# Kernel optimization log

Hardware: AMD Instinct MI355X
Metric: run time of the kernel (lower is better)

The kernel has to match this reference:

```python
import jax, jax.numpy as jnp
import numpy as np

N, C, K, P, Q, PS = 32, 128, 128, 64, 64, 3

def setup_inputs() -> dict:
    key = jax.random.key(0)
    k1, k2, k3 = jax.random.split(key, 3)
    x = jax.random.normal(k1, (N, C, P, Q), dtype=jnp.float32)
    W = jax.random.normal(k2, (K, C * PS * PS), dtype=jnp.float32) * (1.0 / np.sqrt(C * PS * PS))
    perturbs = jax.random.normal(k3, (N, K, P, Q), dtype=jnp.float32)
    return {"x": x, "W": W, "perturbs": perturbs}

def reference(x, W, perturbs):
    # patchify (pad=1, unfold 3x3, stride 1) + matmul with W^T is exactly a
    # 3x3 SAME convolution: flatten order of patchify is (C, kh, kw), matching
    # conv.weight.reshape(k, -1). Express it as a direct conv (no im2col blowup).
    k = W.shape[0]
    c = x.shape[1]
    w = W.reshape(k, c, PS, PS)  # OIHW
    out = jax.lax.conv_general_dilated(
        x, w,
        window_strides=(1, 1),
        padding=((1, 1), (1, 1)),
        dimension_numbers=("NCHW", "OIHW", "NCHW"),
    )
    return out + perturbs
```

## Files before the change

### kernel.cpp

```cpp
#include <hip/hip_runtime.h>
#include <hip/hip_bf16.h>

#define NN 32
#define CCH 128
#define KK 128
#define PP 64
#define QQ 64

typedef __bf16 bf16x8 __attribute__((ext_vector_type(8)));
typedef float f32x16 __attribute__((ext_vector_type(16)));
typedef float f32x4 __attribute__((ext_vector_type(4)));

#define XT_ELEMS (32ull * 64 * 64 * 128)

__global__ __launch_bounds__(256) void prep_x(const float* __restrict__ x,
                                              __bf16* __restrict__ xT) {
    __shared__ float tile[128 * 64];
    const int t = threadIdx.x;
    const int p = blockIdx.x;
    const int n = blockIdx.y;

#pragma unroll
    for (int pass = 0; pass < 8; ++pass) {
        int idx = pass * 256 + t;
        int qf = idx & 15;
        int c  = idx >> 4;
        f32x4 v = *(const f32x4*)(x + (((size_t)n * CCH + c) * PP + p) * QQ + qf * 4);
        int key = ((c >> 3) & 15) * 4;
        *(f32x4*)(tile + c * 64 + ((qf * 4) ^ key)) = v;
    }
    __syncthreads();

#pragma unroll
    for (int pass = 0; pass < 4; ++pass) {
        int cc   = pass * 2 + (t >> 7);
        int rem  = t & 127;
        int q    = rem >> 1;
        int half = rem & 1;
        int c0   = cc * 16 + half * 8;
        int key  = ((c0 >> 3) & 15) * 4;
        bf16x8 o;
#pragma unroll
        for (int j = 0; j < 8; ++j) o[j] = (__bf16)tile[(c0 + j) * 64 + (q ^ key)];
        *(bf16x8*)(xT + ((((size_t)n * 8 + cc) * PP + p) * QQ + q) * 16 + half * 8) = o;
    }
}

__global__ __launch_bounds__(256) void prep_w(const float* __restrict__ W,
                                              __bf16* __restrict__ Wf) {
    const int id = blockIdx.x * 256 + threadIdx.x;
    const int lane = id & 63;
    const int r1   = id >> 6;
    const int kb   = r1 & 3;
    const int r2   = r1 >> 2;
    const int t    = r2 % 9;
    const int cc   = r2 / 9;

    const int k  = kb * 32 + (lane & 31);
    const int c0 = cc * 16 + (lane >> 5) * 8;

    bf16x8 o;
#pragma unroll
    for (int j = 0; j < 8; ++j)
        o[j] = (__bf16)W[(size_t)k * (CCH * 9) + (size_t)(c0 + j) * 9 + t];
    ((bf16x8*)Wf)[id] = o;
}

__global__ __launch_bounds__(256, 2) void conv_main(const __bf16* __restrict__ xT,
                                                    const __bf16* __restrict__ Wf,
                                                    const float* __restrict__ per,
                                                    float* __restrict__ out) {
    __shared__ __align__(16) char scr_lds[4][4096];

    const int tid  = threadIdx.x;
    const int lane = tid & 63;
    const int w    = tid >> 6;
    const int kbs  = w & 1;
    const int pb   = w >> 1;
    const int n    = blockIdx.y;
    const int p0   = blockIdx.x * 4;
    const int m    = lane & 31;
    const int half = lane >> 5;

    bf16x8 bz;
#pragma unroll
    for (int j = 0; j < 8; ++j) bz[j] = (__bf16)0.f;

    f32x16 acc[2][2][2];
#pragma unroll
    for (int a = 0; a < 2; ++a)
#pragma unroll
        for (int b = 0; b < 2; ++b)
#pragma unroll
            for (int c = 0; c < 2; ++c)
#pragma unroll
                for (int e = 0; e < 16; ++e) acc[a][b][c][e] = 0.f;

    const char* xb = (const char*)xT + ((size_t)n * 8) * PP * QQ * 32;

    const bf16x8* wg = (const bf16x8*)Wf + kbs * 128 + lane;

    auto compute = [&](int cc) {
        const char* xcc = xb + (size_t)cc * (PP * QQ * 32);
        const bf16x8* wc = wg + (size_t)cc * 2304;

        bf16x8 a_cur[3][2], a_prev[3][2];
#pragma unroll
        for (int ri = 0; ri < 4; ++ri) {
            const int r  = p0 + pb * 2 + ri - 1;
            const bool rok = ((unsigned)r < (unsigned)PP);

            bf16x8 b[3][2];
            if (rok) {
                const char* xrow = xcc + (size_t)r * 2048 + half * 16;
#pragma unroll
                for (int dq = 0; dq < 3; ++dq)
#pragma unroll
                    for (int qb = 0; qb < 2; ++qb) {
                        int q_in = qb * 32 + m + dq - 1;
                        bool ok  = ((unsigned)q_in < (unsigned)QQ);
                        int qc   = ok ? q_in : 0;
                        bf16x8 v = *(const bf16x8*)(xrow + qc * 32);
                        b[dq][qb] = ok ? v : bz;
                    }
            }

            if (ri < 3) {
#pragma unroll
                for (int dq = 0; dq < 3; ++dq)
#pragma unroll
                    for (int kb = 0; kb < 2; ++kb)
                        a_cur[dq][kb] = wc[((ri * 3 + dq) * 4 + kb) * 64];
            }

            if (rok) {
                if (ri >= 1) {
#pragma unroll
                    for (int dq = 0; dq < 3; ++dq)
#pragma unroll
                        for (int kb = 0; kb < 2; ++kb)
#pragma unroll
                            for (int qb = 0; qb < 2; ++qb)
                                acc[1][kb][qb] = __builtin_amdgcn_mfma_f32_32x32x16_bf16(
                                    a_prev[dq][kb], b[dq][qb], acc[1][kb][qb], 0, 0, 0);
                }
                if (ri < 3) {
#pragma unroll
                    for (int dq = 0; dq < 3; ++dq)
#pragma unroll
                        for (int kb = 0; kb < 2; ++kb)
#pragma unroll
                            for (int qb = 0; qb < 2; ++qb)
                                acc[0][kb][qb] = __builtin_amdgcn_mfma_f32_32x32x16_bf16(
                                    a_cur[dq][kb], b[dq][qb], acc[0][kb][qb], 0, 0, 0);
                }
            }

            if (ri < 3) {
#pragma unroll
                for (int dq = 0; dq < 3; ++dq)
#pragma unroll
                    for (int kb = 0; kb < 2; ++kb) a_prev[dq][kb] = a_cur[dq][kb];
            }
        }
    };

    for (int cc = 0; cc < 7; ++cc) compute(cc);

    auto tile_addr = [&](int it, int j) -> size_t {
        int oi = it >> 2, kbi = (it >> 1) & 1, qb = it & 1;
        int prow = p0 + pb * 2 + oi;
        int k = (kbs * 2 + kbi) * 32 + (lane >> 3) + j * 8;
        int q = qb * 32 + (lane & 7) * 4;
        return (((size_t)n * KK + k) * PP + prow) * QQ + q;
    };

    float* scr = (float*)scr_lds[w];

    auto process = [&](int it, f32x4 (&pv)[4]) {
        int oi = it >> 2, kbi = (it >> 1) & 1, qb = it & 1;
        f32x16 v = acc[oi][kbi][qb];
#pragma unroll
        for (int r = 0; r < 16; ++r) {
            int kl = (r & 3) + 8 * (r >> 2) + 4 * half;
            scr[kl * 32 + ((((m >> 2) ^ (kl & 7)) << 2) | (m & 3))] = v[r];
        }
#pragma unroll
        for (int j = 0; j < 4; ++j) {
            int kl = (lane >> 3) + j * 8;
            f32x4 d = *(const f32x4*)(scr + kl * 32 + (((lane & 7) ^ (kl & 7)) << 2));
            f32x4 s = d + pv[j];
            __builtin_nontemporal_store(s, (f32x4*)(out + tile_addr(it, j)));
        }
    };

    f32x4 pv0[4], pv1[4];
#pragma unroll
    for (int j = 0; j < 4; ++j) pv0[j] = *(const f32x4*)(per + tile_addr(0, j));

    compute(7);

#pragma unroll
    for (int itp = 0; itp < 4; ++itp) {
        const int itA = itp * 2, itB = itp * 2 + 1;
#pragma unroll
        for (int j = 0; j < 4; ++j) pv1[j] = *(const f32x4*)(per + tile_addr(itB, j));
        process(itA, pv0);
        if (itp < 3) {
#pragma unroll
            for (int j = 0; j < 4; ++j)
                pv0[j] = *(const f32x4*)(per + tile_addr(itA + 2, j));
        }
        process(itB, pv1);
    }
}

extern "C" void kernel_launch(void* const* d_in, const int* in_sizes, int n_in,
                              void* d_out, int out_size, void* d_ws, size_t ws_size,
                              hipStream_t stream) {
    const float* x   = (const float*)d_in[0];
    const float* W   = (const float*)d_in[1];
    const float* per = (const float*)d_in[2];
    float* out = (float*)d_out;

    __bf16* xT = (__bf16*)d_ws;
    __bf16* Wf = (__bf16*)((char*)d_ws + XT_ELEMS * 2);

    prep_x<<<dim3(PP, NN), 256, 0, stream>>>(x, xT);
    prep_w<<<dim3(72), 256, 0, stream>>>(W, Wf);
    conv_main<<<dim3(PP / 4, NN), 256, 0, stream>>>(xT, Wf, per, out);
}
```

Baseline: 214.6 us.

## Stage input rows in LDS via async global-to-LDS loads, halve rows per block

The conv kernel now stages four channel chunks of the 4 input rows it needs (with zeroed halo columns) into LDS using global_load_lds, and reads B fragments from LDS instead of with per-lane bounds-checked global loads. Each block now covers 2 output rows instead of 4, so the grid doubles, the per-wave accumulators halve, and occupancy is raised to 3 blocks per CU. The aim is to remove the column-boundary select logic and redundant global traffic and to lower register pressure. In exchange it adds block-wide barriers between staging and compute with no overlap, and the 3-row halo is reloaded for every 2 output rows.

```diff
diff --git a/kernel.cpp b/kernel.cpp
--- a/kernel.cpp
+++ b/kernel.cpp
@@ -66,11 +66,16 @@
     ((bf16x8*)Wf)[id] = o;
 }
 
-__global__ __launch_bounds__(256, 2) void conv_main(const __bf16* __restrict__ xT,
+#define XPITCH 2112
+#define XROWS  4
+#define CC_HALF 4
+#define XLDS_BYTES (CC_HALF * XROWS * XPITCH)
+
+__global__ __launch_bounds__(256, 3) void conv_main(const __bf16* __restrict__ xT,
                                                     const __bf16* __restrict__ Wf,
                                                     const float* __restrict__ per,
                                                     float* __restrict__ out) {
-    __shared__ __align__(16) char scr_lds[4][4096];
+    __shared__ __align__(16) char xlds[XLDS_BYTES];
 
     const int tid  = threadIdx.x;
     const int lane = tid & 63;
@@ -78,108 +83,107 @@
     const int kbs  = w & 1;
     const int pb   = w >> 1;
     const int n    = blockIdx.y;
-    const int p0   = blockIdx.x * 4;
+    const int p0   = blockIdx.x * 2;
     const int m    = lane & 31;
     const int half = lane >> 5;
 
-    bf16x8 bz;
-#pragma unroll
-    for (int j = 0; j < 8; ++j) bz[j] = (__bf16)0.f;
-
-    f32x16 acc[2][2][2];
-#pragma unroll
-    for (int a = 0; a < 2; ++a)
-#pragma unroll
-        for (int b = 0; b < 2; ++b)
-#pragma unroll
-            for (int c = 0; c < 2; ++c)
-#pragma unroll
-                for (int e = 0; e < 16; ++e) acc[a][b][c][e] = 0.f;
+    if (tid < 64) {
+        int row = tid >> 2, part = tid & 3;
+        int off = row * XPITCH + (part >> 1) * 2080 + (part & 1) * 16;
+        *(f32x4*)(xlds + off) = f32x4{0.f, 0.f, 0.f, 0.f};
+    }
+
+    f32x16 acc[2][2];
+#pragma unroll
+    for (int b = 0; b < 2; ++b)
+#pragma unroll
+        for (int c = 0; c < 2; ++c)
+#pragma unroll
+            for (int e = 0; e < 16; ++e) acc[b][c][e] = 0.f;
 
     const char* xb = (const char*)xT + ((size_t)n * 8) * PP * QQ * 32;
 
+    auto stage4 = [&](int ccb) {
+#pragma unroll
+        for (int it = 0; it < 8; ++it) {
+            int id  = it * 256 + tid;
+            int cc4 = id >> 9;
+            int rem = id & 511;
+            int row = rem >> 7;
+            int wi  = (rem & 127) * 16;
+            int r   = p0 - 1 + row;
+            int rc  = r < 0 ? 0 : (r > 63 ? 63 : r);
+            __builtin_amdgcn_global_load_lds(
+                (const __attribute__((address_space(1))) unsigned int*)
+                    (xb + (size_t)(ccb + cc4) * 131072 + (size_t)rc * 2048 + wi),
+                (__attribute__((address_space(3))) unsigned int*)
+                    (xlds + (cc4 * XROWS + row) * XPITCH + 32 + wi),
+                16, 0, 0);
+        }
+    };
+
     const bf16x8* wg = (const bf16x8*)Wf + kbs * 128 + lane;
 
-    auto compute = [&](int cc) {
-        const char* xcc = xb + (size_t)cc * (PP * QQ * 32);
+    auto compute = [&](int slot, int cc) {
+        const char* xbase = xlds + slot * (XROWS * XPITCH);
         const bf16x8* wc = wg + (size_t)cc * 2304;
 
-        bf16x8 a_cur[3][2], a_prev[3][2];
-#pragma unroll
-        for (int ri = 0; ri < 4; ++ri) {
-            const int r  = p0 + pb * 2 + ri - 1;
+#pragma unroll
+        for (int ri = 0; ri < 3; ++ri) {
+            const int r = p0 + pb + ri - 1;
             const bool rok = ((unsigned)r < (unsigned)PP);
-
-            bf16x8 b[3][2];
             if (rok) {
-                const char* xrow = xcc + (size_t)r * 2048 + half * 16;
+                const char* rbase = xbase + (pb + ri) * XPITCH + half * 16;
+                bf16x8 b[3][2], a[3][2];
 #pragma unroll
                 for (int dq = 0; dq < 3; ++dq)
 #pragma unroll
-                    for (int qb = 0; qb < 2; ++qb) {
-                        int q_in = qb * 32 + m + dq - 1;
-                        bool ok  = ((unsigned)q_in < (unsigned)QQ);
-                        int qc   = ok ? q_in : 0;
-                        bf16x8 v = *(const bf16x8*)(xrow + qc * 32);
-                        b[dq][qb] = ok ? v : bz;
-                    }
+                    for (int qb = 0; qb < 2; ++qb)
+                        b[dq][qb] = *(const bf16x8*)(rbase + (qb * 32 + m + dq) * 32);
+#pragma unroll
+                for (int dq = 0; dq < 3; ++dq)
+#pragma unroll
+                    for (int kb = 0; kb < 2; ++kb)
+                        a[dq][kb] = wc[((ri * 3 + dq) * 4 + kb) * 64];
+#pragma unroll
+                for (int dq = 0; dq < 3; ++dq)
+#pragma unroll
+                    for (int kb = 0; kb < 2; ++kb)
+#pragma unroll
+                        for (int qb = 0; qb < 2; ++qb)
+                            acc[kb][qb] = __builtin_amdgcn_mfma_f32_32x32x16_bf16(
+                                a[dq][kb], b[dq][qb], acc[kb][qb], 0, 0, 0);
             }
-
-            if (ri < 3) {
-#pragma unroll
-                for (int dq = 0; dq < 3; ++dq)
-#pragma unroll
-                    for (int kb = 0; kb < 2; ++kb)
-                        a_cur[dq][kb] = wc[((ri * 3 + dq) * 4 + kb) * 64];
-            }
-
-            if (rok) {
-                if (ri >= 1) {
-#pragma unroll
-                    for (int dq = 0; dq < 3; ++dq)
-#pragma unroll
-                        for (int kb = 0; kb < 2; ++kb)
-#pragma unroll
-                            for (int qb = 0; qb < 2; ++qb)
-                                acc[1][kb][qb] = __builtin_amdgcn_mfma_f32_32x32x16_bf16(
-                                    a_prev[dq][kb], b[dq][qb], acc[1][kb][qb], 0, 0, 0);
-                }
-                if (ri < 3) {
-#pragma unroll
-                    for (int dq = 0; dq < 3; ++dq)
-#pragma unroll
-                        for (int kb = 0; kb < 2; ++kb)
-#pragma unroll
-                            for (int qb = 0; qb < 2; ++qb)
-                                acc[0][kb][qb] = __builtin_amdgcn_mfma_f32_32x32x16_bf16(
-                                    a_cur[dq][kb], b[dq][qb], acc[0][kb][qb], 0, 0, 0);
-                }
-            }
-
-            if (ri < 3) {
-#pragma unroll
-                for (int dq = 0; dq < 3; ++dq)
-#pragma unroll
-                    for (int kb = 0; kb < 2; ++kb) a_prev[dq][kb] = a_cur[dq][kb];
-            }
-        }
-    };
-
-    for (int cc = 0; cc < 7; ++cc) compute(cc);
+        }
+    };
+
+    stage4(0);
+    __syncthreads();
+    compute(0, 0); compute(1, 1); compute(2, 2); compute(3, 3);
+    __syncthreads();
+    stage4(4);
+    __syncthreads();
+    compute(0, 4); compute(1, 5); compute(2, 6);
 
     auto tile_addr = [&](int it, int j) -> size_t {
-        int oi = it >> 2, kbi = (it >> 1) & 1, qb = it & 1;
-        int prow = p0 + pb * 2 + oi;
-        int k = (kbs * 2 + kbi) * 32 + (lane >> 3) + j * 8;
+        int kb = it >> 1, qb = it & 1;
+        int k = kbs * 64 + kb * 32 + (lane >> 3) + j * 8;
         int q = qb * 32 + (lane & 7) * 4;
-        return (((size_t)n * KK + k) * PP + prow) * QQ + q;
-    };
-
-    float* scr = (float*)scr_lds[w];
+        return (((size_t)n * KK + k) * PP + (p0 + pb)) * QQ + q;
+    };
+
+    f32x4 pv0[4], pv1[4];
+#pragma unroll
+    for (int j = 0; j < 4; ++j) pv0[j] = *(const f32x4*)(per + tile_addr(0, j));
+
+    compute(3, 7);
+
+    __syncthreads();
+    float* scr = (float*)(xlds + w * 4096);
 
     auto process = [&](int it, f32x4 (&pv)[4]) {
-        int oi = it >> 2, kbi = (it >> 1) & 1, qb = it & 1;
-        f32x16 v = acc[oi][kbi][qb];
+        int kb = it >> 1, qb = it & 1;
+        f32x16 v = acc[kb][qb];
 #pragma unroll
         for (int r = 0; r < 16; ++r) {
             int kl = (r & 3) + 8 * (r >> 2) + 4 * half;
@@ -194,19 +198,13 @@
         }
     };
 
-    f32x4 pv0[4], pv1[4];
-#pragma unroll
-    for (int j = 0; j < 4; ++j) pv0[j] = *(const f32x4*)(per + tile_addr(0, j));
-
-    compute(7);
-
-#pragma unroll
-    for (int itp = 0; itp < 4; ++itp) {
+#pragma unroll
+    for (int itp = 0; itp < 2; ++itp) {
         const int itA = itp * 2, itB = itp * 2 + 1;
 #pragma unroll
         for (int j = 0; j < 4; ++j) pv1[j] = *(const f32x4*)(per + tile_addr(itB, j));
         process(itA, pv0);
-        if (itp < 3) {
+        if (itp < 1) {
 #pragma unroll
             for (int j = 0; j < 4; ++j)
                 pv0[j] = *(const f32x4*)(per + tile_addr(itA + 2, j));
@@ -228,5 +226,5 @@
 
     prep_x<<<dim3(PP, NN), 256, 0, stream>>>(x, xT);
     prep_w<<<dim3(72), 256, 0, stream>>>(W, Wf);
-    conv_main<<<dim3(PP / 4, NN), 256, 0, stream>>>(xT, Wf, per, out);
-}
+    conv_main<<<dim3(PP / 2, NN), 256, 0, stream>>>(xT, Wf, per, out);
+}
```

Result: no change. 214.4 us (-0.1%).
